# Kernel tuning notes

Measured on AMD Instinct MI355X. Metric: run time of the kernel, lower is better.

Reference implementation:

```python
import jax, jax.numpy as jnp
import numpy as np

B, N, C = 16, 2048, 128
NCLS = 40


def setup_inputs() -> dict:
    key = jax.random.key(0)
    ks = iter(jax.random.split(key, 40))

    def nrm(shape, s=0.05):
        return jax.random.normal(next(ks), shape, dtype=jnp.float32) * s

    return {
        "x": jax.random.normal(next(ks), (B, 3, N), dtype=jnp.float32),
        "conv1_w": nrm((128, 3), 0.5),
        "bn1_g": jnp.ones((128,), jnp.float32), "bn1_b": jnp.zeros((128,), jnp.float32),
        "conv2_w": nrm((128, 128)),
        "bn2_g": jnp.ones((128,), jnp.float32), "bn2_b": jnp.zeros((128,), jnp.float32),
        "sa_wqk": nrm((4, 32, 128)),
        "sa_wv": nrm((4, 128, 128)), "sa_bv": nrm((4, 128)),
        "sa_wt": nrm((4, 128, 128)), "sa_bt": nrm((4, 128)),
        "sa_g": jnp.ones((4, 128), jnp.float32), "sa_b": jnp.zeros((4, 128), jnp.float32),
        "fuse_w": nrm((1024, 512)),
        "fuse_g": jnp.ones((1024,), jnp.float32), "fuse_b": jnp.zeros((1024,), jnp.float32),
        "lin1_w": nrm((512, 1024)),
        "bn6_g": jnp.ones((512,), jnp.float32), "bn6_b": jnp.zeros((512,), jnp.float32),
        "lin2_w": nrm((256, 512)), "lin2_b": jnp.zeros((256,), jnp.float32),
        "bn7_g": jnp.ones((256,), jnp.float32), "bn7_b": jnp.zeros((256,), jnp.float32),
        "lin3_w": nrm((NCLS, 256)), "lin3_b": jnp.zeros((NCLS,), jnp.float32),
    }


def _pconv(w, x):
    # 1x1 Conv1d == channel matmul: [O,C] x [B,C,N] -> [B,O,N]
    return jnp.einsum('oc,bcn->bon', w, x)


def _fwd(x, conv1_w, bn1_g, bn1_b, conv2_w, bn2_g, bn2_b,
         sa_wqk, sa_wv, sa_bv, sa_wt, sa_bt, sa_g, sa_b,
         fuse_w, fuse_g, fuse_b, lin1_w, bn6_g, bn6_b,
         lin2_w, lin2_b, bn7_g, bn7_b, lin3_w, lin3_b):
    # conv stem (BN in eval mode: running mean=0, var=1 -> affine)
    h = jax.nn.relu(bn1_g[:, None] * _pconv(conv1_w, x) + bn1_b[:, None])
    h = jax.nn.relu(bn2_g[:, None] * _pconv(conv2_w, h) + bn2_b[:, None])

    outs = []
    for i in range(4):  # fixed number of structurally identical SA blocks
        # q_conv and k_conv share the same weight (aliased in the torch code)
        q = jnp.einsum('dc,bcn->bdn', sa_wqk[i], h)           # [B,32,N]
        energy = jnp.einsum('bdi,bdj->bij', q, q)             # [B,N,N]
        att = jax.nn.softmax(energy, axis=-1)
        att = att / (1e-9 + att.sum(axis=1, keepdims=True))   # extra L1 renorm over dim=1
        v = _pconv(sa_wv[i], h) + sa_bv[i][:, None]           # [B,C,N]
        x_r = jnp.einsum('bcn,bnm->bcm', v, att)              # [B,C,N]
        t = _pconv(sa_wt[i], h - x_r) + sa_bt[i][:, None]
        h = h + jax.nn.relu(sa_g[i][:, None] * t + sa_b[i][:, None])
        outs.append(h)

    cat = jnp.concatenate(outs, axis=1)                        # [B,512,N]
    f = fuse_g[:, None] * _pconv(fuse_w, cat) + fuse_b[:, None]
    f = jnp.where(f > 0, f, 0.2 * f)                           # LeakyReLU(0.2)
    g = f.max(axis=-1)                                         # adaptive max pool -> [B,1024]

    h1 = jax.nn.relu(bn6_g * (g @ lin1_w.T) + bn6_b)           # dropout = identity (eval)
    h2 = jax.nn.relu(bn7_g * (h1 @ lin2_w.T + lin2_b) + bn7_b)
    return h2 @ lin3_w.T + lin3_b                              # [B,40]


def reference(x, conv1_w, bn1_g, bn1_b, conv2_w, bn2_g, bn2_b,
              sa_wqk, sa_wv, sa_bv, sa_wt, sa_bt, sa_g, sa_b,
              fuse_w, fuse_g, fuse_b, lin1_w, bn6_g, bn6_b,
              lin2_w, lin2_b, bn7_g, bn7_b, lin3_w, lin3_b):
    return _fwd(x, conv1_w, bn1_g, bn1_b, conv2_w, bn2_g, bn2_b,
                sa_wqk, sa_wv, sa_bv, sa_wt, sa_bt, sa_g, sa_b,
                fuse_w, fuse_g, fuse_b, lin1_w, bn6_g, bn6_b,
                lin2_w, lin2_b, bn7_g, bn7_b, lin3_w, lin3_b)
```

## Files before the change

### kernel.cpp

```cpp
#include <hip/hip_runtime.h>

typedef __attribute__((ext_vector_type(4))) float f4;
typedef __attribute__((ext_vector_type(8))) short s16x8;
typedef __attribute__((ext_vector_type(4))) unsigned short us4;
typedef __attribute__((ext_vector_type(2))) unsigned int u32x2;
typedef unsigned short u16;
typedef unsigned int u32;

#define DEVI __device__ __forceinline__

DEVI u16 f2bf(float f){
    u32 u = __builtin_bit_cast(u32, f);
    u32 r = (u + 0x7fffu + ((u >> 16) & 1u)) >> 16;
    return (u16)r;
}
DEVI f4 mfma16(s16x8 a, s16x8 b, f4 c){
    return __builtin_amdgcn_mfma_f32_16x16x32_bf16(a, b, c, 0, 0, 0);
}
DEVI u32 cvtpk(float lo, float hi){
    u32 r;
    asm("v_cvt_pk_bf16_f32 %0, %1, %2" : "=v"(r) : "v"(lo), "v"(hi));
    return r;
}
DEVI void gload(const u16* g, u16* l){
    __builtin_amdgcn_global_load_lds((const __attribute__((address_space(1))) void*)g,
                                     (__attribute__((address_space(3))) void*)l, 16, 0, 0);
}

#define L2E 1.44269504088896340736f

__global__ __launch_bounds__(256) void k_cast(const float* w2, const float* wqk,
                                              const float* wv, const float* wt,
                                              const float* wf, u16* out){
    int i = blockIdx.x * 256 + threadIdx.x;
    if(i < 16384)       out[i] = f2bf(w2[i]);
    else if(i < 32768)  out[i] = f2bf(wqk[i - 16384]);
    else if(i < 98304)  out[i] = f2bf(wv[i - 32768]);
    else if(i < 163840) out[i] = f2bf(wt[i - 98304]);
    else if(i < 688128){
        int t = i - 163840;
        int o = t >> 9, c = t & 511;
        int jg = o >> 4, l15 = o & 15, ks = c >> 5, kr = c & 31;
        out[163840 + (size_t)(jg*16 + ks)*512 + ((kr>>3)*16 + l15)*8 + (kr&7)] = f2bf(wf[t]);
    }
}

__global__ __launch_bounds__(256) void k_stem1(const float* x, const float* w1,
                                               const float* g1, const float* b1, u16* h1tb){
    int t = blockIdx.x * 256 + threadIdx.x;
    int b = t >> 11, n = t & 2047;
    const float* xb = x + (size_t)b * 3 * 2048 + n;
    float x0 = xb[0], x1 = xb[2048], x2 = xb[4096];
    u32* o = (u32*)(h1tb + (size_t)t * 128);
    #pragma unroll 8
    for(int c = 0; c < 128; c += 2){
        float a0 = fmaxf(g1[c]   * (w1[c*3+0]*x0 + w1[c*3+1]*x1 + w1[c*3+2]*x2) + b1[c],   0.f);
        float a1 = fmaxf(g1[c+1] * (w1[c*3+3]*x0 + w1[c*3+4]*x1 + w1[c*3+5]*x2) + b1[c+1], 0.f);
        o[c >> 1] = (u32)f2bf(a0) | ((u32)f2bf(a1) << 16);
    }
}

DEVI int swz512(int bid){ return ((bid & 7) << 6) | (bid >> 3); }
DEVI int swz1024(int bid){ return ((bid & 7) << 7) | (bid >> 3); }

DEVI void qv_phase(const u16* T, const u16* wqkb, const u16* wvb, const float* bv,
                   u16* qb, u16* vt, int b, int n0, int wv_, int l15, int kg){
    f4 accv[8], accq[2];
    #pragma unroll
    for(int j=0;j<8;j++) accv[j] = (f4){0.f,0.f,0.f,0.f};
    accq[0] = (f4){0.f,0.f,0.f,0.f}; accq[1] = accq[0];
    int row = wv_*16 + l15;
    #pragma unroll
    for(int ks=0; ks<4; ks++){
        s16x8 a = *(const s16x8*)&T[row*128 + ((ks*32 + kg*8) ^ ((row&7)<<3))];
        #pragma unroll
        for(int j=0;j<8;j++){
            s16x8 bb = *(const s16x8*)(wvb + (size_t)(j*16 + l15)*128 + ks*32 + kg*8);
            accv[j] = mfma16(a, bb, accv[j]);
        }
        #pragma unroll
        for(int f=0; f<2; f++){
            s16x8 wf_ = *(const s16x8*)(wqkb + (size_t)(f*16 + l15)*128 + ks*32 + kg*8);
            accq[f] = mfma16(wf_, a, accq[f]);
        }
    }
    int nb = n0 + wv_*16;
    int it = nb >> 5;
    int k0 = (nb & 31) + kg*4;
    int vbase = ((k0 >> 3)*16)*8 + (k0 & 7);
    #pragma unroll
    for(int j=0;j<8;j++){
        float bvo = bv[j*16 + l15];
        us4 pk;
        #pragma unroll
        for(int r=0;r<4;r++) pk[r] = f2bf(accv[j][r] + bvo);
        *(us4*)(vt + (size_t)((b*64 + it)*8 + j)*512 + vbase + l15*8) = pk;
    }
    int n = n0 + wv_*16 + l15;
    #pragma unroll
    for(int f=0; f<2; f++){
        us4 pk;
        #pragma unroll
        for(int r=0;r<4;r++) pk[r] = f2bf(accq[f][r]);
        *(us4*)(qb + (size_t)(b*2048 + n)*32 + f*16 + kg*4) = pk;
    }
}

__global__ __launch_bounds__(256) void k_conv2qv(const u16* h1tb, const u16* w2b,
                                                 const float* g2, const float* b2,
                                                 float* ht0,
                                                 const u16* wqkb, const u16* wvb,
                                                 const float* bv, u16* qb, u16* vt){
    __shared__ u16 T[8192];
    int bid2 = swz512(blockIdx.x);
    int b = bid2 >> 5;
    int n0 = (bid2 & 31) << 6;
    int lane = threadIdx.x & 63, wv_ = threadIdx.x >> 6;
    int l15 = lane & 15, kg = lane >> 4;
    const u16* arow = h1tb + (size_t)(b*2048 + n0 + wv_*16 + l15) * 128 + kg*8;
    f4 acc[8];
    #pragma unroll
    for(int j=0;j<8;j++) acc[j] = (f4){0.f,0.f,0.f,0.f};
    #pragma unroll
    for(int ks=0; ks<4; ks++){
        s16x8 a = *(const s16x8*)(arow + ks*32);
        #pragma unroll
        for(int j=0;j<8;j++){
            s16x8 bb = *(const s16x8*)(w2b + (size_t)(j*16 + l15)*128 + ks*32 + kg*8);
            acc[j] = mfma16(a, bb, acc[j]);
        }
    }
    int nn0 = n0 + wv_*16 + kg*4;
    #pragma unroll
    for(int j=0;j<8;j++){
        int o = j*16 + l15;
        float gg = g2[o], be = b2[o];
        #pragma unroll
        for(int r=0;r<4;r++){
            float h = fmaxf(gg * acc[j][r] + be, 0.f);
            int nl = wv_*16 + kg*4 + r;
            ht0[(size_t)(b*2048 + nn0 + r) * 128 + o] = h;
            T[nl*128 + (o ^ ((nl&7)<<3))] = f2bf(h);
        }
    }
    __syncthreads();
    qv_phase(T, wqkb, wvb, bv, qb, vt, b, n0, wv_, l15, kg);
}

__global__ __launch_bounds__(256) void k_passA(const u16* qb, float* crowp){
    int bid2 = swz1024(blockIdx.x);
    int b = bid2 >> 6;
    int rest = bid2 & 63;
    int i0 = (rest >> 1) << 6;
    int jh = rest & 1;
    int jbeg = jh << 10;
    int lane = threadIdx.x & 63, wv_ = threadIdx.x >> 6;
    int l15 = lane & 15, kg = lane >> 4;
    const u16* qbase = qb + (size_t)b * 2048 * 32;
    s16x8 af = *(const s16x8*)(qbase + (size_t)(i0 + wv_*16 + l15)*32 + kg*8);
    float m[4], s[4], mml[4];
    const f4 z = {0.f,0.f,0.f,0.f};
    {
        s16x8 b0 = *(const s16x8*)(qbase + (size_t)(jbeg + l15)*32 + kg*8);
        s16x8 b1 = *(const s16x8*)(qbase + (size_t)(jbeg + 16 + l15)*32 + kg*8);
        f4 e0 = mfma16(af, b0, z);
        f4 e1 = mfma16(af, b1, z);
        #pragma unroll
        for(int r=0;r<4;r++){
            m[r] = fmaxf(e0[r], e1[r]);
            mml[r] = -m[r]*L2E;
            s[r] = exp2f(fmaf(e0[r], L2E, mml[r])) + exp2f(fmaf(e1[r], L2E, mml[r]));
        }
    }
    for(int j0=jbeg+32; j0<jbeg+1024; j0+=32){
        s16x8 b0 = *(const s16x8*)(qbase + (size_t)(j0 + l15)*32 + kg*8);
        s16x8 b1 = *(const s16x8*)(qbase + (size_t)(j0 + 16 + l15)*32 + kg*8);
        f4 e0 = mfma16(af, b0, z);
        f4 e1 = mfma16(af, b1, z);
        #pragma unroll
        for(int r=0;r<4;r++){
            float mx = fmaxf(e0[r], e1[r]);
            if(mx > m[r] + 8.f){
                s[r] *= exp2f((m[r]-mx)*L2E);
                m[r] = mx; mml[r] = -mx*L2E;
            }
            s[r] += exp2f(fmaf(e0[r], L2E, mml[r])) + exp2f(fmaf(e1[r], L2E, mml[r]));
        }
    }
    #pragma unroll
    for(int d=1; d<16; d<<=1){
        #pragma unroll
        for(int r=0;r<4;r++){
            float mo = __shfl_xor(m[r], d);
            float so = __shfl_xor(s[r], d);
            float mn = fmaxf(m[r], mo);
            s[r] = s[r]*exp2f((m[r]-mn)*L2E) + so*exp2f((mo-mn)*L2E);
            m[r] = mn;
        }
    }
    if(l15 == 0){
        #pragma unroll
        for(int r=0;r<4;r++){
            int i = i0 + wv_*16 + kg*4 + r;
            crowp[jh*32768 + b*2048 + i] = m[r]*L2E + log2f(s[r]);
        }
    }
}

__global__ __launch_bounds__(512) void k_passBT(const u16* qb, const u16* vt,
                                                const float* crowp,
                                                const float* hprev, int ldh,
                                                const u16* wtb, const float* bt,
                                                const float* sg, const float* sb,
                                                float* catf_o, u16* catb_o,
                                                const u16* wqkb2, const u16* wvb2,
                                                const float* bv2,
                                                u16* qb2, u16* vt2, int doQV){
    __shared__ __align__(16) char SB[58368];
    u16*   V   = (u16*)SB;
    u16*   P   = (u16*)(SB + 32768);
    float* CR  = (float*)(SB + 49152);
    float* csl = (float*)(SB + 57344);
    int bid2 = swz512(blockIdx.x);
    int b = bid2 >> 5;
    int j0 = (bid2 & 31) << 6;
    int tid = threadIdx.x;
    int lane = tid & 63, wv_ = tid >> 6;
    int jw = wv_ >> 2, ih = (wv_ >> 1) & 1, jcH = wv_ & 1;
    int l15 = lane & 15, kg = lane >> 4;
    int jh = jw * 32;
    int pairOff = (jw*2 + ih) * 1024;
    int isub = ih*2 + jcH;
    const u16* qbase = qb + (size_t)b * 2048 * 32;
    const u16* vtb = vt + (size_t)b * 64*8*512;

    #pragma unroll
    for(int p=0;p<4;p++){
        int i = p*512 + tid;
        float c0 = crowp[b*2048 + i], c1 = crowp[32768 + b*2048 + i];
        float mx = fmaxf(c0, c1), mn = fminf(c0, c1);
        CR[i] = mx + log2f(1.f + exp2f(mn - mx));
    }

    s16x8 eb0 = *(const s16x8*)(qbase + (size_t)(j0 + jh + l15)*32 + kg*8);
    s16x8 eb1 = *(const s16x8*)(qbase + (size_t)(j0 + jh + 16 + l15)*32 + kg*8);
    f4 acc[2][4];
    #pragma unroll
    for(int jb=0;jb<2;jb++)
        #pragma unroll
        for(int jj=0;jj<4;jj++) acc[jb][jj] = (f4){0.f,0.f,0.f,0.f};
    float csp0 = 0.f, csp1 = 0.f;
    const f4 z = {0.f,0.f,0.f,0.f};

    auto stage = [&](int ic, int buf){
        const u16* src = vtb + (size_t)ic*8192 + wv_*1024 + lane*8;
        u16* dst = V + buf*8192 + wv_*1024;
        gload(src, dst);
        gload(src + 512, dst + 512);
    };
    auto eph = [&](int ic, int buf){
        s16x8 ea = *(const s16x8*)(qbase + (size_t)(ic*64 + isub*16 + l15)*32 + kg*8);
        f4 cc = *(const f4*)&CR[ic*64 + isub*16 + kg*4];
        int wbase = buf*4096 + pairOff + ((jcH*2 + (kg>>1))*16 + l15)*8 + (kg&1)*4;
        {
            f4 e = mfma16(ea, eb0, z);
            float q0 = exp2f(fmaf(e[0], L2E, -cc[0]));
            float q1 = exp2f(fmaf(e[1], L2E, -cc[1]));
            float q2 = exp2f(fmaf(e[2], L2E, -cc[2]));
            float q3 = exp2f(fmaf(e[3], L2E, -cc[3]));
            csp0 += q0 + q1 + q2 + q3;
            u32x2 pk = { cvtpk(q0, q1), cvtpk(q2, q3) };
            *(u32x2*)&P[wbase] = pk;
        }
        {
            f4 e = mfma16(ea, eb1, z);
            float q0 = exp2f(fmaf(e[0], L2E, -cc[0]));
            float q1 = exp2f(fmaf(e[1], L2E, -cc[1]));
            float q2 = exp2f(fmaf(e[2], L2E, -cc[2]));
            float q3 = exp2f(fmaf(e[3], L2E, -cc[3]));
            csp1 += q0 + q1 + q2 + q3;
            u32x2 pk = { cvtpk(q0, q1), cvtpk(q2, q3) };
            *(u32x2*)&P[wbase + 512] = pk;
        }
    };

    __syncthreads();
    stage(0, 0);
    eph(0, 0);
    __syncthreads();
    for(int it=0; it<32; it++){
        int cur = it & 1;
        if(it < 31){ stage(it+1, cur^1); eph(it+1, cur^1); }
        s16x8 pa0 = *(const s16x8*)&P[cur*4096 + pairOff + lane*8];
        s16x8 pa1 = *(const s16x8*)&P[cur*4096 + pairOff + 512 + lane*8];
        __builtin_amdgcn_s_setprio(1);
        #pragma unroll
        for(int jj=0;jj<4;jj++){
            s16x8 vf = *(const s16x8*)&V[cur*8192 + ih*4096 + (jcH*4 + jj)*512 + lane*8];
            acc[0][jj] = mfma16(pa0, vf, acc[0][jj]);
            acc[1][jj] = mfma16(pa1, vf, acc[1][jj]);
        }
        __builtin_amdgcn_s_setprio(0);
        __syncthreads();
    }
    csp0 += __shfl_xor(csp0, 16); csp0 += __shfl_xor(csp0, 32);
    csp1 += __shfl_xor(csp1, 16); csp1 += __shfl_xor(csp1, 32);
    if(lane < 16){
        int g = ih*2 + jcH;
        csl[g*64 + jh + l15]      = csp0;
        csl[g*64 + jh + 16 + l15] = csp1;
    }
    __syncthreads();
    float* comb = (float*)SB;
    if(ih == 1){
        #pragma unroll
        for(int jb=0;jb<2;jb++)
            #pragma unroll
            for(int jj=0;jj<4;jj++)
                *(f4*)&comb[(jw*2+jcH)*2048 + (jb*4+jj)*256 + lane*4] = acc[jb][jj];
    }
    __syncthreads();
    u16* Td = (u16*)(SB + 32768);
    if(ih == 0){
        #pragma unroll
        for(int jb=0;jb<2;jb++)
            #pragma unroll
            for(int jj=0;jj<4;jj++){
                f4 o = *(const f4*)&comb[(jw*2+jcH)*2048 + (jb*4+jj)*256 + lane*4];
                acc[jb][jj][0] += o[0]; acc[jb][jj][1] += o[1];
                acc[jb][jj][2] += o[2]; acc[jb][jj][3] += o[3];
            }
        #pragma unroll
        for(int jb=0;jb<2;jb++)
            #pragma unroll
            for(int r=0;r<4;r++){
                int jr = jh + jb*16 + kg*4 + r;
                float inv = 1.0f / (1e-9f + csl[jr] + csl[64+jr] + csl[128+jr] + csl[192+jr]);
                int n = j0 + jr;
                const float* hrow = hprev + (size_t)(b*2048 + n)*ldh;
                #pragma unroll
                for(int jj=0;jj<4;jj++){
                    int c = (jcH*4 + jj)*16 + l15;
                    Td[jr*128 + (c ^ ((jr&7)<<3))] = f2bf(hrow[c] - acc[jb][jj][r]*inv);
                }
            }
    }
    __syncthreads();
    int jw2 = wv_ >> 1, ih2 = wv_ & 1;
    int jh2 = jw2 * 16;
    f4 accT[4];
    #pragma unroll
    for(int j2=0;j2<4;j2++) accT[j2] = (f4){0.f,0.f,0.f,0.f};
    {
        int arow_l = jh2 + l15;
        #pragma unroll
        for(int ks=0; ks<4; ks++){
            s16x8 a = *(const s16x8*)&Td[arow_l*128 + ((ks*32 + kg*8) ^ ((arow_l&7)<<3))];
            #pragma unroll
            for(int j2=0;j2<4;j2++){
                int o = ih2*64 + j2*16 + l15;
                s16x8 bb = *(const s16x8*)(wtb + (size_t)o*128 + ks*32 + kg*8);
                accT[j2] = mfma16(a, bb, accT[j2]);
            }
        }
    }
    u16* T2 = (u16*)SB;
    #pragma unroll
    for(int j2=0;j2<4;j2++){
        int o = ih2*64 + j2*16 + l15;
        float bto = bt[o], gg = sg[o], be = sb[o];
        #pragma unroll
        for(int r=0;r<4;r++){
            int jr = jh2 + kg*4 + r;
            int n = j0 + jr;
            float t = accT[j2][r] + bto;
            float hv = hprev[(size_t)(b*2048 + n)*ldh + o];
            float hn = hv + fmaxf(gg*t + be, 0.f);
            size_t oi = (size_t)(b*2048 + n)*512 + o;
            u16 hb = f2bf(hn);
            catf_o[oi] = hn;
            catb_o[oi] = hb;
            T2[jr*128 + (o ^ ((jr&7)<<3))] = hb;
        }
    }
    __syncthreads();
    if(doQV){
        f4 accv[4], accq;
        #pragma unroll
        for(int jj=0;jj<4;jj++) accv[jj] = (f4){0.f,0.f,0.f,0.f};
        accq = (f4){0.f,0.f,0.f,0.f};
        int row = jh2 + l15;
        #pragma unroll
        for(int ks=0; ks<4; ks++){
            s16x8 a = *(const s16x8*)&T2[row*128 + ((ks*32 + kg*8) ^ ((row&7)<<3))];
            #pragma unroll
            for(int jj=0;jj<4;jj++){
                s16x8 bb = *(const s16x8*)(wvb2 + (size_t)((ih2*4+jj)*16 + l15)*128 + ks*32 + kg*8);
                accv[jj] = mfma16(a, bb, accv[jj]);
            }
            s16x8 wf_ = *(const s16x8*)(wqkb2 + (size_t)(ih2*16 + l15)*128 + ks*32 + kg*8);
            accq = mfma16(wf_, a, accq);
        }
        int nb = j0 + jh2;
        int it2 = nb >> 5;
        int k0 = (nb & 31) + kg*4;
        int vbase = ((k0 >> 3)*16)*8 + (k0 & 7);
        #pragma unroll
        for(int jj=0;jj<4;jj++){
            int jc4 = ih2*4 + jj;
            float bvo = bv2[jc4*16 + l15];
            us4 pk;
            #pragma unroll
            for(int r=0;r<4;r++) pk[r] = f2bf(accv[jj][r] + bvo);
            *(us4*)(vt2 + (size_t)((b*64 + it2)*8 + jc4)*512 + vbase + l15*8) = pk;
        }
        int n = j0 + jh2 + l15;
        us4 pk;
        #pragma unroll
        for(int r=0;r<4;r++) pk[r] = f2bf(accq[r]);
        *(us4*)(qb2 + (size_t)(b*2048 + n)*32 + ih2*16 + kg*4) = pk;
    }
}

__global__ __launch_bounds__(512) void k_fuse(const u16* catb, const u16* wft,
                                              const float* fg, const float* fb, float* gpart){
    __shared__ u16 AB[24576];
    __shared__ float red[512];
    int bid2 = swz1024(blockIdx.x);
    int b  = bid2 >> 6;
    int rest = bid2 & 63;
    int ng = rest >> 2;
    int og = rest & 3;
    int tid = threadIdx.x;
    int lane = tid & 63, wv_ = tid >> 6;
    int wn = wv_ >> 2, wo = wv_ & 3;
    int l15 = lane & 15, kg = lane >> 4;

    f4 acc[4][4];
    #pragma unroll
    for(int mi=0;mi<4;mi++)
        #pragma unroll
        for(int j=0;j<4;j++) acc[mi][j] = (f4){0.f,0.f,0.f,0.f};

    for(int ksc=0; ksc<8; ksc++){
        if(ksc) __syncthreads();
        #pragma unroll
        for(int q=0;q<2;q++){
            int s = wv_*128 + q*64 + lane;
            int r = s >> 3;
            int c16 = (s & 7) ^ (r & 7);
            const u16* g = catb + (size_t)(b*2048 + ng*128 + r)*512 + ksc*64 + c16*8;
            gload(g, &AB[wv_*1024 + q*512]);
        }
        #pragma unroll
        for(int q=0;q<4;q++){
            int p = wv_*4 + q;
            int jgl = p >> 1, ksl = p & 1;
            const u16* g = wft + (size_t)((og*16 + jgl)*16 + ksc*2 + ksl)*512 + lane*8;
            gload(g, &AB[8192 + p*512]);
        }
        __syncthreads();
        #pragma unroll
        for(int ks=0; ks<2; ks++){
            s16x8 av[4], bw[4];
            #pragma unroll
            for(int mi=0;mi<4;mi++){
                int row = wn*64 + mi*16 + l15;
                av[mi] = *(const s16x8*)&AB[row*64 + ((ks*32 + kg*8) ^ ((row&7)<<3))];
            }
            #pragma unroll
            for(int j=0;j<4;j++){
                int p = (wo*4 + j)*2 + ks;
                bw[j] = *(const s16x8*)&AB[8192 + p*512 + lane*8];
            }
            #pragma unroll
            for(int j=0;j<4;j++)
                #pragma unroll
                for(int mi=0;mi<4;mi++)
                    acc[mi][j] = mfma16(av[mi], bw[j], acc[mi][j]);
        }
    }
    float vmax[4];
    #pragma unroll
    for(int j=0;j<4;j++){
        int o = og*256 + wo*64 + j*16 + l15;
        float fgv = fg[o], fbv = fb[o];
        float vm = -1e30f;
        #pragma unroll
        for(int mi=0;mi<4;mi++)
            #pragma unroll
            for(int r=0;r<4;r++){
                float f = fgv*acc[mi][j][r] + fbv;
                f = (f > 0.f) ? f : 0.2f*f;
                vm = fmaxf(vm, f);
            }
        vm = fmaxf(vm, __shfl_xor(vm, 16));
        vm = fmaxf(vm, __shfl_xor(vm, 32));
        vmax[j] = vm;
    }
    if(lane < 16){
        #pragma unroll
        for(int j=0;j<4;j++) red[(wo*2 + wn)*64 + j*16 + lane] = vmax[j];
    }
    __syncthreads();
    if(tid < 256){
        int wo2 = tid >> 6, ol = tid & 63;
        float m = fmaxf(red[(wo2*2+0)*64 + ol], red[(wo2*2+1)*64 + ol]);
        gpart[(size_t)(ng*16 + b)*1024 + og*256 + wo2*64 + ol] = m;
    }
}

__global__ __launch_bounds__(256) void k_gmax(const float* gpart, float* g){
    int i = blockIdx.x*256 + threadIdx.x;
    float m = gpart[i];
    #pragma unroll
    for(int p=1;p<16;p++) m = fmaxf(m, gpart[(size_t)p*16384 + i]);
    g[i] = m;
}

__global__ __launch_bounds__(256) void k_mlp(const float* in, const float* W, const float* bias,
                                             const float* gm, const float* bt, float* out,
                                             int IN, int OUT, int dorelu){
    int wid = blockIdx.x*4 + (threadIdx.x >> 6);
    int lane = threadIdx.x & 63;
    int b = wid / OUT, o = wid - b*OUT;
    if(b >= 16) return;
    const f4* ir = (const f4*)(in + (size_t)b*IN);
    const f4* wr = (const f4*)(W + (size_t)o*IN);
    float s = 0.f;
    for(int k=lane; k < (IN>>2); k += 64){
        f4 a = ir[k], w = wr[k];
        s += a[0]*w[0] + a[1]*w[1] + a[2]*w[2] + a[3]*w[3];
    }
    #pragma unroll
    for(int d=1; d<64; d<<=1) s += __shfl_xor(s, d);
    if(lane == 0){
        if(bias) s += bias[o];
        if(gm) s = gm[o]*s + bt[o];
        if(dorelu) s = fmaxf(s, 0.f);
        out[(size_t)b*OUT + o] = s;
    }
}

constexpr size_t MB = 1048576;
constexpr size_t OFF_WB   = 0;
constexpr size_t OFF_H1TB = 2*MB;
constexpr size_t OFF_HT0  = 10*MB;
constexpr size_t OFF_QB0  = 26*MB;
constexpr size_t OFF_QB1  = 28*MB;
constexpr size_t OFF_VB0  = 30*MB;
constexpr size_t OFF_VB1  = 38*MB;
constexpr size_t OFF_CROW = 46*MB;
constexpr size_t OFF_GP   = 46*MB + 262144;
constexpr size_t OFF_CATF = 48*MB;
constexpr size_t OFF_CATB = 112*MB;
constexpr size_t OFF_G    = 144*MB;
constexpr size_t OFF_H1V  = OFF_G + 65536;
constexpr size_t OFF_H2V  = OFF_H1V + 32768;

extern "C" void kernel_launch(void* const* d_in, const int* in_sizes, int n_in,
                              void* d_out, int out_size, void* d_ws, size_t ws_size,
                              hipStream_t stream){
    const float* x       = (const float*)d_in[0];
    const float* conv1_w = (const float*)d_in[1];
    const float* bn1_g   = (const float*)d_in[2];
    const float* bn1_b   = (const float*)d_in[3];
    const float* conv2_w = (const float*)d_in[4];
    const float* bn2_g   = (const float*)d_in[5];
    const float* bn2_b   = (const float*)d_in[6];
    const float* sa_wqk  = (const float*)d_in[7];
    const float* sa_wv   = (const float*)d_in[8];
    const float* sa_bv   = (const float*)d_in[9];
    const float* sa_wt   = (const float*)d_in[10];
    const float* sa_bt   = (const float*)d_in[11];
    const float* sa_g    = (const float*)d_in[12];
    const float* sa_b    = (const float*)d_in[13];
    const float* fuse_w  = (const float*)d_in[14];
    const float* fuse_g  = (const float*)d_in[15];
    const float* fuse_b  = (const float*)d_in[16];
    const float* lin1_w  = (const float*)d_in[17];
    const float* bn6_g   = (const float*)d_in[18];
    const float* bn6_b   = (const float*)d_in[19];
    const float* lin2_w  = (const float*)d_in[20];
    const float* lin2_b  = (const float*)d_in[21];
    const float* bn7_g   = (const float*)d_in[22];
    const float* bn7_b   = (const float*)d_in[23];
    const float* lin3_w  = (const float*)d_in[24];
    const float* lin3_b  = (const float*)d_in[25];

    char* ws = (char*)d_ws;
    u16*   wb    = (u16*)(ws + OFF_WB);
    u16*   h1tb  = (u16*)(ws + OFF_H1TB);
    float* ht0   = (float*)(ws + OFF_HT0);
    u16*   qbb[2] = { (u16*)(ws + OFF_QB0), (u16*)(ws + OFF_QB1) };
    u16*   vtb[2] = { (u16*)(ws + OFF_VB0), (u16*)(ws + OFF_VB1) };
    float* crowp = (float*)(ws + OFF_CROW);
    float* gpart = (float*)(ws + OFF_GP);
    float* catf  = (float*)(ws + OFF_CATF);
    u16*   catb  = (u16*)(ws + OFF_CATB);
    float* gbuf  = (float*)(ws + OFF_G);
    float* h1v   = (float*)(ws + OFF_H1V);
    float* h2v   = (float*)(ws + OFF_H2V);

    k_cast <<<2688, 256, 0, stream>>>(conv2_w, sa_wqk, sa_wv, sa_wt, fuse_w, wb);
    k_stem1<<<128,  256, 0, stream>>>(x, conv1_w, bn1_g, bn1_b, h1tb);
    k_conv2qv<<<512, 256, 0, stream>>>(h1tb, wb, bn2_g, bn2_b, ht0,
                                       wb + 16384, wb + 32768, sa_bv, qbb[0], vtb[0]);

    for(int blk = 0; blk < 4; blk++){
        int cur = blk & 1, nxt = cur ^ 1;
        const float* hprev = (blk == 0) ? ht0 : (catf + (size_t)(blk-1)*128);
        int          ldh   = (blk == 0) ? 128 : 512;
        const u16* wtb  = wb + 98304 + blk*16384;
        int nb2 = (blk < 3) ? (blk + 1) : 3;
        const u16* wqkb2 = wb + 16384 + nb2*4096;
        const u16* wvb2  = wb + 32768 + nb2*16384;

        k_passA<<<1024, 256, 0, stream>>>(qbb[cur], crowp);
        k_passBT<<<512, 512, 0, stream>>>(qbb[cur], vtb[cur], crowp, hprev, ldh,
                                          wtb, sa_bt + blk*128, sa_g + blk*128, sa_b + blk*128,
                                          catf + (size_t)blk*128, catb + (size_t)blk*128,
                                          wqkb2, wvb2, sa_bv + nb2*128,
                                          qbb[nxt], vtb[nxt], (blk < 3) ? 1 : 0);
    }

    k_fuse<<<1024, 512, 0, stream>>>(catb, wb + 163840, fuse_g, fuse_b, gpart);
    k_gmax<<<64,   256, 0, stream>>>(gpart, gbuf);
    k_mlp <<<2048, 256, 0, stream>>>(gbuf, lin1_w, nullptr, bn6_g, bn6_b, h1v, 1024, 512, 1);
    k_mlp <<<1024, 256, 0, stream>>>(h1v, lin2_w, lin2_b, bn7_g, bn7_b, h2v, 512, 256, 1);
    k_mlp <<<160,  256, 0, stream>>>(h2v, lin3_w, lin3_b, nullptr, nullptr,
                                     (float*)d_out, 256, 40, 0);
}
```

Measured before the change: 448.7 us.

## Store residual activations in bf16 only and split softmax row pass into quarters

```diff
diff --git a/kernel.cpp b/kernel.cpp
--- a/kernel.cpp
+++ b/kernel.cpp
@@ -13,6 +13,10 @@
     u32 u = __builtin_bit_cast(u32, f);
     u32 r = (u + 0x7fffu + ((u >> 16) & 1u)) >> 16;
     return (u16)r;
+}
+DEVI float bf2f(u16 h){
+    u32 u = ((u32)h) << 16;
+    return __builtin_bit_cast(float, u);
 }
 DEVI f4 mfma16(s16x8 a, s16x8 b, f4 c){
     return __builtin_amdgcn_mfma_f32_16x16x32_bf16(a, b, c, 0, 0, 0);
@@ -62,6 +66,7 @@
 
 DEVI int swz512(int bid){ return ((bid & 7) << 6) | (bid >> 3); }
 DEVI int swz1024(int bid){ return ((bid & 7) << 7) | (bid >> 3); }
+DEVI int swz2048(int bid){ return ((bid & 7) << 8) | (bid >> 3); }
 
 DEVI void qv_phase(const u16* T, const u16* wqkb, const u16* wvb, const float* bv,
                    u16* qb, u16* vt, int b, int n0, int wv_, int l15, int kg){
@@ -108,7 +113,7 @@
 
 __global__ __launch_bounds__(256) void k_conv2qv(const u16* h1tb, const u16* w2b,
                                                  const float* g2, const float* b2,
-                                                 float* ht0,
+                                                 u16* htb,
                                                  const u16* wqkb, const u16* wvb,
                                                  const float* bv, u16* qb, u16* vt){
     __shared__ u16 T[8192];
@@ -139,8 +144,9 @@
         for(int r=0;r<4;r++){
             float h = fmaxf(gg * acc[j][r] + be, 0.f);
             int nl = wv_*16 + kg*4 + r;
-            ht0[(size_t)(b*2048 + nn0 + r) * 128 + o] = h;
-            T[nl*128 + (o ^ ((nl&7)<<3))] = f2bf(h);
+            u16 hb = f2bf(h);
+            htb[(size_t)(b*2048 + nn0 + r) * 128 + o] = hb;
+            T[nl*128 + (o ^ ((nl&7)<<3))] = hb;
         }
     }
     __syncthreads();
@@ -148,12 +154,12 @@
 }
 
 __global__ __launch_bounds__(256) void k_passA(const u16* qb, float* crowp){
-    int bid2 = swz1024(blockIdx.x);
-    int b = bid2 >> 6;
-    int rest = bid2 & 63;
-    int i0 = (rest >> 1) << 6;
-    int jh = rest & 1;
-    int jbeg = jh << 10;
+    int bid2 = swz2048(blockIdx.x);
+    int b = bid2 >> 7;
+    int rest = bid2 & 127;
+    int i0 = (rest >> 2) << 6;
+    int jq = rest & 3;
+    int jbeg = jq << 9;
     int lane = threadIdx.x & 63, wv_ = threadIdx.x >> 6;
     int l15 = lane & 15, kg = lane >> 4;
     const u16* qbase = qb + (size_t)b * 2048 * 32;
@@ -172,7 +178,7 @@
             s[r] = exp2f(fmaf(e0[r], L2E, mml[r])) + exp2f(fmaf(e1[r], L2E, mml[r]));
         }
     }
-    for(int j0=jbeg+32; j0<jbeg+1024; j0+=32){
+    for(int j0=jbeg+32; j0<jbeg+512; j0+=32){
         s16x8 b0 = *(const s16x8*)(qbase + (size_t)(j0 + l15)*32 + kg*8);
         s16x8 b1 = *(const s16x8*)(qbase + (size_t)(j0 + 16 + l15)*32 + kg*8);
         f4 e0 = mfma16(af, b0, z);
@@ -202,17 +208,17 @@
         #pragma unroll
         for(int r=0;r<4;r++){
             int i = i0 + wv_*16 + kg*4 + r;
-            crowp[jh*32768 + b*2048 + i] = m[r]*L2E + log2f(s[r]);
+            crowp[jq*32768 + b*2048 + i] = m[r]*L2E + log2f(s[r]);
         }
     }
 }
 
 __global__ __launch_bounds__(512) void k_passBT(const u16* qb, const u16* vt,
                                                 const float* crowp,
-                                                const float* hprev, int ldh,
+                                                const u16* hprev, int ldh,
                                                 const u16* wtb, const float* bt,
                                                 const float* sg, const float* sb,
-                                                float* catf_o, u16* catb_o,
+                                                u16* catb_o,
                                                 const u16* wqkb2, const u16* wvb2,
                                                 const float* bv2,
                                                 u16* qb2, u16* vt2, int doQV){
@@ -237,9 +243,11 @@
     #pragma unroll
     for(int p=0;p<4;p++){
         int i = p*512 + tid;
-        float c0 = crowp[b*2048 + i], c1 = crowp[32768 + b*2048 + i];
-        float mx = fmaxf(c0, c1), mn = fminf(c0, c1);
-        CR[i] = mx + log2f(1.f + exp2f(mn - mx));
+        float c0 = crowp[b*2048 + i],          c1 = crowp[32768 + b*2048 + i];
+        float c2 = crowp[65536 + b*2048 + i],  c3 = crowp[98304 + b*2048 + i];
+        float mx = fmaxf(fmaxf(c0, c1), fmaxf(c2, c3));
+        float sum = exp2f(c0 - mx) + exp2f(c1 - mx) + exp2f(c2 - mx) + exp2f(c3 - mx);
+        CR[i] = mx + log2f(sum);
     }
 
     s16x8 eb0 = *(const s16x8*)(qbase + (size_t)(j0 + jh + l15)*32 + kg*8);
@@ -337,11 +345,11 @@
                 int jr = jh + jb*16 + kg*4 + r;
                 float inv = 1.0f / (1e-9f + csl[jr] + csl[64+jr] + csl[128+jr] + csl[192+jr]);
                 int n = j0 + jr;
-                const float* hrow = hprev + (size_t)(b*2048 + n)*ldh;
+                const u16* hrow = hprev + (size_t)(b*2048 + n)*ldh;
                 #pragma unroll
                 for(int jj=0;jj<4;jj++){
                     int c = (jcH*4 + jj)*16 + l15;
-                    Td[jr*128 + (c ^ ((jr&7)<<3))] = f2bf(hrow[c] - acc[jb][jj][r]*inv);
+                    Td[jr*128 + (c ^ ((jr&7)<<3))] = f2bf(bf2f(hrow[c]) - acc[jb][jj][r]*inv);
                 }
             }
     }
@@ -374,12 +382,10 @@
             int jr = jh2 + kg*4 + r;
             int n = j0 + jr;
             float t = accT[j2][r] + bto;
-            float hv = hprev[(size_t)(b*2048 + n)*ldh + o];
+            float hv = bf2f(hprev[(size_t)(b*2048 + n)*ldh + o]);
             float hn = hv + fmaxf(gg*t + be, 0.f);
-            size_t oi = (size_t)(b*2048 + n)*512 + o;
             u16 hb = f2bf(hn);
-            catf_o[oi] = hn;
-            catb_o[oi] = hb;
+            catb_o[(size_t)(b*2048 + n)*512 + o] = hb;
             T2[jr*128 + (o ^ ((jr&7)<<3))] = hb;
         }
     }
@@ -545,14 +551,13 @@
 constexpr size_t MB = 1048576;
 constexpr size_t OFF_WB   = 0;
 constexpr size_t OFF_H1TB = 2*MB;
-constexpr size_t OFF_HT0  = 10*MB;
+constexpr size_t OFF_HTB  = 10*MB;
 constexpr size_t OFF_QB0  = 26*MB;
 constexpr size_t OFF_QB1  = 28*MB;
 constexpr size_t OFF_VB0  = 30*MB;
 constexpr size_t OFF_VB1  = 38*MB;
 constexpr size_t OFF_CROW = 46*MB;
-constexpr size_t OFF_GP   = 46*MB + 262144;
-constexpr size_t OFF_CATF = 48*MB;
+constexpr size_t OFF_GP   = 46*MB + 524288;
 constexpr size_t OFF_CATB = 112*MB;
 constexpr size_t OFF_G    = 144*MB;
 constexpr size_t OFF_H1V  = OFF_G + 65536;
@@ -591,12 +596,11 @@
     char* ws = (char*)d_ws;
     u16*   wb    = (u16*)(ws + OFF_WB);
     u16*   h1tb  = (u16*)(ws + OFF_H1TB);
-    float* ht0   = (float*)(ws + OFF_HT0);
+    u16*   htb   = (u16*)(ws + OFF_HTB);
     u16*   qbb[2] = { (u16*)(ws + OFF_QB0), (u16*)(ws + OFF_QB1) };
     u16*   vtb[2] = { (u16*)(ws + OFF_VB0), (u16*)(ws + OFF_VB1) };
     float* crowp = (float*)(ws + OFF_CROW);
     float* gpart = (float*)(ws + OFF_GP);
-    float* catf  = (float*)(ws + OFF_CATF);
     u16*   catb  = (u16*)(ws + OFF_CATB);
     float* gbuf  = (float*)(ws + OFF_G);
     float* h1v   = (float*)(ws + OFF_H1V);
@@ -604,22 +608,22 @@
 
     k_cast <<<2688, 256, 0, stream>>>(conv2_w, sa_wqk, sa_wv, sa_wt, fuse_w, wb);
     k_stem1<<<128,  256, 0, stream>>>(x, conv1_w, bn1_g, bn1_b, h1tb);
-    k_conv2qv<<<512, 256, 0, stream>>>(h1tb, wb, bn2_g, bn2_b, ht0,
+    k_conv2qv<<<512, 256, 0, stream>>>(h1tb, wb, bn2_g, bn2_b, htb,
                                        wb + 16384, wb + 32768, sa_bv, qbb[0], vtb[0]);
 
     for(int blk = 0; blk < 4; blk++){
         int cur = blk & 1, nxt = cur ^ 1;
-        const float* hprev = (blk == 0) ? ht0 : (catf + (size_t)(blk-1)*128);
-        int          ldh   = (blk == 0) ? 128 : 512;
+        const u16* hprev = (blk == 0) ? htb : (catb + (size_t)(blk-1)*128);
+        int        ldh   = (blk == 0) ? 128 : 512;
         const u16* wtb  = wb + 98304 + blk*16384;
         int nb2 = (blk < 3) ? (blk + 1) : 3;
         const u16* wqkb2 = wb + 16384 + nb2*4096;
         const u16* wvb2  = wb + 32768 + nb2*16384;
 
-        k_passA<<<1024, 256, 0, stream>>>(qbb[cur], crowp);
+        k_passA<<<2048, 256, 0, stream>>>(qbb[cur], crowp);
         k_passBT<<<512, 512, 0, stream>>>(qbb[cur], vtb[cur], crowp, hprev, ldh,
                                           wtb, sa_bt + blk*128, sa_g + blk*128, sa_b + blk*128,
-                                          catf + (size_t)blk*128, catb + (size_t)blk*128,
+                                          catb + (size_t)blk*128,
                                           wqkb2, wvb2, sa_bv + nb2*128,
                                           qbb[nxt], vtb[nxt], (blk < 3) ? 1 : 0);
     }
```

After: 555.6 us. 1.24x slower.
